# Optimization experiments

Hardware: AMD Instinct MI355X
Metric: run time of the kernel (lower is better)

The kernel has to match this reference:

```python
import jax, jax.numpy as jnp
import numpy as np

D_MODEL = 1024
N_HEADS = 16
D_KV = 64
B, S = 2, 2048


def setup_inputs() -> dict:
    key = jax.random.key(0)
    ks = jax.random.split(key, 7)
    scale = 1.0 / np.sqrt(D_MODEL)
    return {
        "query": jax.random.normal(ks[0], (B, S, D_MODEL), jnp.float32),
        "key": jax.random.normal(ks[1], (B, S, D_MODEL), jnp.float32),
        "value": jax.random.normal(ks[2], (B, S, D_MODEL), jnp.float32),
        "mask": jnp.zeros((B, 1, 1, S), jnp.float32),
        "Wq": jax.random.normal(ks[3], (D_MODEL, N_HEADS * D_KV), jnp.float32) * scale,
        "Wk": jax.random.normal(ks[4], (D_MODEL, N_HEADS * D_KV), jnp.float32) * scale,
        "Wv": jax.random.normal(ks[5], (D_MODEL, N_HEADS * D_KV), jnp.float32) * scale,
        "Wo": jax.random.normal(ks[6], (N_HEADS * D_KV, D_MODEL), jnp.float32) * scale,
    }


def _split_heads(x):
    b, s, _ = x.shape
    return x.reshape(b, s, N_HEADS, D_KV).transpose(0, 2, 1, 3)  # [B,H,S,Dk]


def reference(query, key, value, mask, Wq, Wk, Wv, Wo):
    q = _split_heads(query @ Wq)
    k = _split_heads(key @ Wk)
    v = _split_heads(value @ Wv)
    scores = jnp.einsum("bhqd,bhkd->bhqk", q, k) / jnp.sqrt(
        jnp.asarray(D_KV, scores_dtype := q.dtype)
    )
    scores = scores + mask
    attn = jax.nn.softmax(scores, axis=-1)  # dropout_rate=0 -> identity
    ctx = jnp.einsum("bhqk,bhkd->bhqd", attn, v)
    ctx = ctx.transpose(0, 2, 1, 3).reshape(query.shape[0], -1, N_HEADS * D_KV)
    hidden = ctx @ Wo
    return hidden
```

## Files before the change

kernel.cpp:

```cpp
#include <hip/hip_runtime.h>
#include <hip/hip_bf16.h>
#include <stdint.h>

typedef __bf16 bf16;
typedef __bf16 bf16x8 __attribute__((ext_vector_type(8)));
typedef __bf16 bf16x4 __attribute__((ext_vector_type(4)));
typedef float  f32x4  __attribute__((ext_vector_type(4)));
typedef float  f32x16 __attribute__((ext_vector_type(16)));

#define S_LEN  2048
#define NH     16
#define DKV    64
#define DMODEL 1024
#define LOG2E  1.4426950408889634f

__device__ __forceinline__ void async_load16(const void* g, void* l) {
  __builtin_amdgcn_global_load_lds(
      (const __attribute__((address_space(1))) uint32_t*)(uintptr_t)g,
      (__attribute__((address_space(3))) uint32_t*)(uintptr_t)l,
      16, 0, 0);
}

__global__ void transpose_w(const float* __restrict__ W0, const float* __restrict__ W1,
                            const float* __restrict__ W2, const float* __restrict__ W3,
                            bf16* __restrict__ T0, bf16* __restrict__ T1,
                            bf16* __restrict__ T2, bf16* __restrict__ T3)
{
  int z = blockIdx.z;
  const float* W = (z == 0) ? W0 : (z == 1) ? W1 : (z == 2) ? W2 : W3;
  bf16* T = (z == 0) ? T0 : (z == 1) ? T1 : (z == 2) ? T2 : T3;
  __shared__ float tile[32][33];
  int n0 = blockIdx.x * 32, k0 = blockIdx.y * 32;
  int tx = threadIdx.x, ty = threadIdx.y;
  for (int i = 0; i < 32; i += 8)
    tile[ty + i][tx] = W[(size_t)(k0 + ty + i) * DMODEL + n0 + tx];
  __syncthreads();
  for (int i = 0; i < 32; i += 8)
    T[(size_t)(n0 + ty + i) * DMODEL + k0 + tx] = (bf16)tile[tx][ty + i];
}

__global__ __launch_bounds__(256) void gemm_qkv(
    const float* __restrict__ Aq, const float* __restrict__ Ak, const float* __restrict__ Av,
    const bf16* __restrict__ Bq, const bf16* __restrict__ Bk, const bf16* __restrict__ Bv,
    bf16* __restrict__ Cq, bf16* __restrict__ Ck, bf16* __restrict__ Cv)
{
  __shared__ __align__(16) char smem[64 * 132 * 2];
  bf16* As = (bf16*)smem;
  bf16* Bs = (bf16*)smem + 128 * 32;
  bf16* Ls = (bf16*)smem;

  const int z = blockIdx.z;
  const float* A = (z == 0) ? Aq : (z == 1) ? Ak : Av;
  const bf16* Bt = (z == 0) ? Bq : (z == 1) ? Bk : Bv;
  bf16* C        = (z == 0) ? Cq : (z == 1) ? Ck : Cv;

  const int m0 = blockIdx.x * 128;
  const int n0 = blockIdx.y * 128;
  const int tid = threadIdx.x;
  const int lane = tid & 63;
  const int wave = tid >> 6;
  const int wm = (wave >> 1) * 64;
  const int wn = (wave & 1) * 64;
  const int row = lane & 15;
  const int quad = lane >> 4;

  f32x4 acc[4][4];
  for (int i = 0; i < 4; ++i)
    for (int j = 0; j < 4; ++j) acc[i][j] = (f32x4){0.f, 0.f, 0.f, 0.f};

  const int ar = tid >> 2;
  const int ac8 = (tid & 3) * 8;

  for (int kt = 0; kt < 32; ++kt) {
    const int kk = kt << 5;
    const float* s0p = A + (size_t)(m0 + ar) * DMODEL + kk + ac8;
    const float* s1p = s0p + (size_t)64 * DMODEL;
    f32x4 a00 = *(const f32x4*)s0p;
    f32x4 a01 = *(const f32x4*)(s0p + 4);
    f32x4 a10 = *(const f32x4*)s1p;
    f32x4 a11 = *(const f32x4*)(s1p + 4);
    __syncthreads();
    for (int j = 0; j < 2; ++j) {
      int base = j * 256 + wave * 64;
      int idx = base + lane;
      int r = idx >> 2;
      int cb = (idx & 3) << 4;
      async_load16((const char*)(Bt + (size_t)(n0 + r) * DMODEL + kk) + cb,
                   (char*)Bs + (size_t)base * 16);
    }
    bf16x8 o0, o1;
    for (int u = 0; u < 4; ++u) { o0[u] = (bf16)a00[u]; o0[u + 4] = (bf16)a01[u]; }
    for (int u = 0; u < 4; ++u) { o1[u] = (bf16)a10[u]; o1[u + 4] = (bf16)a11[u]; }
    *(bf16x8*)(As + ar * 32 + ac8) = o0;
    *(bf16x8*)(As + (ar + 64) * 32 + ac8) = o1;
    __syncthreads();
    bf16x8 af[4], bfr[4];
    for (int i = 0; i < 4; ++i)
      af[i] = *(const bf16x8*)(As + (wm + i * 16 + row) * 32 + quad * 8);
    for (int j = 0; j < 4; ++j)
      bfr[j] = *(const bf16x8*)(Bs + (wn + j * 16 + row) * 32 + quad * 8);
    for (int i = 0; i < 4; ++i)
      for (int j = 0; j < 4; ++j)
        acc[i][j] = __builtin_amdgcn_mfma_f32_16x16x32_bf16(af[i], bfr[j], acc[i][j], 0, 0, 0);
  }

  if (z != 2) {
    const int bq = m0 >> 11;
    for (int p = 0; p < 2; ++p) {
      __syncthreads();
      if ((wave >> 1) == p) {
        for (int i = 0; i < 4; ++i)
          for (int j = 0; j < 4; ++j)
            for (int r = 0; r < 4; ++r)
              Ls[(i * 16 + quad * 4 + r) * 132 + wn + j * 16 + row] = (bf16)acc[i][j][r];
      }
      __syncthreads();
      for (int u = 0; u < 4; ++u) {
        int cc = u * 256 + tid;
        int rloc = cc >> 4, c8 = (cc & 15) * 8;
        int s = (m0 + p * 64 + rloc) & 2047;
        int gn = n0 + c8;
        int h = gn >> 6, d = gn & 63;
        bf16x8 val = *(const bf16x8*)(Ls + rloc * 132 + c8);
        *(bf16x8*)(C + (((size_t)(bq * NH + h)) * S_LEN + s) * DKV + d) = val;
      }
    }
  } else {
    for (int i = 0; i < 4; ++i)
      for (int j = 0; j < 4; ++j) {
        int gm = m0 + wm + i * 16 + quad * 4;
        int gn = n0 + wn + j * 16 + row;
        int b = gm >> 11, s = gm & 2047;
        int h = gn >> 6,  d = gn & 63;
        int bh = b * NH + h;
        int tile = s >> 6, kb = (s & 63) >> 2;
        bf16x4 t;
        for (int r = 0; r < 4; ++r) t[r] = (bf16)acc[i][j][r];
        *(bf16x4*)(C + ((((size_t)bh * 32 + tile) * 16 + kb) * 64 + d) * 4) = t;
      }
  }
}

__global__ __launch_bounds__(256, 4) void attn_kernel(
    const bf16* __restrict__ Qh, const bf16* __restrict__ Kh, const bf16* __restrict__ Vperm,
    const float* __restrict__ mask, float* __restrict__ Opart, float* __restrict__ Lpart)
{
  __shared__ __align__(16) bf16 Ks[64 * 64];
  __shared__ __align__(16) bf16 Vts[64 * 64];
  __shared__ __align__(16) float masks2[64];

  const int bh = blockIdx.x;
  const int b = bh >> 4;
  const int q0 = blockIdx.y * 128;
  const int zh = blockIdx.z;
  const int tid = threadIdx.x;
  const int lane = tid & 63;
  const int wave = tid >> 6;
  const int ln = lane & 31;
  const int hi = lane >> 5;
  const float SC2 = 0.125f * LOG2E;

  const int qg = q0 + wave * 32 + ln;
  bf16x8 qf[4];
  {
    const bf16* qrow = Qh + ((size_t)bh * S_LEN + qg) * DKV;
    for (int c = 0; c < 4; ++c)
      qf[c] = *(const bf16x8*)(qrow + c * 16 + hi * 8);
  }

  f32x16 O[2];
  for (int nb = 0; nb < 2; ++nb)
    for (int i = 0; i < 16; ++i) O[nb][i] = 0.f;
  float lsum = 0.f;

  for (int it = 0; it < 16; ++it) {
    const int kv0 = zh * 1024 + it * 64;
    __syncthreads();
    const bf16* vtile = Vperm + ((size_t)bh * 32 + (kv0 >> 6)) * 4096;
    for (int j = 0; j < 2; ++j) {
      int base = j * 256 + wave * 64;
      int idx = base + lane;
      int r = idx >> 3;
      int cc = (idx & 7) ^ (r & 7);
      async_load16(Kh + ((size_t)bh * S_LEN + kv0 + r) * DKV + cc * 8,
                   (char*)Ks + (size_t)base * 16);
      async_load16(vtile + (size_t)idx * 8,
                   (char*)Vts + (size_t)base * 16);
    }
    if (tid < 64) masks2[tid] = mask[b * S_LEN + kv0 + tid] * LOG2E;
    __syncthreads();

    f32x16 Sm[2];
    for (int i = 0; i < 16; ++i) { Sm[0][i] = 0.f; Sm[1][i] = 0.f; }
    for (int c = 0; c < 4; ++c) {
      bf16x8 k0 = *(const bf16x8*)(Ks + ln * 64        + (((2 * c + hi) ^ (ln & 7)) << 3));
      bf16x8 k1 = *(const bf16x8*)(Ks + (32 + ln) * 64 + (((2 * c + hi) ^ (ln & 7)) << 3));
      Sm[0] = __builtin_amdgcn_mfma_f32_32x32x16_bf16(k0, qf[c], Sm[0], 0, 0, 0);
      Sm[1] = __builtin_amdgcn_mfma_f32_32x32x16_bf16(k1, qf[c], Sm[1], 0, 0, 0);
    }

    for (int cg = 0; cg < 4; ++cg) {
      int mb = cg >> 1, g = cg & 1;
      int koff = 32 * mb + 16 * g + 4 * hi;
      f32x4 mklo = *(const f32x4*)(masks2 + koff);
      f32x4 mkhi = *(const f32x4*)(masks2 + koff + 8);
      bf16x8 ap;
      float ls0 = 0.f;
      for (int u = 0; u < 4; ++u) {
        float p = __builtin_amdgcn_exp2f(Sm[mb][g * 8 + u] * SC2 + mklo[u]);
        ls0 += p; ap[u] = (bf16)p;
      }
      for (int u = 0; u < 4; ++u) {
        float p = __builtin_amdgcn_exp2f(Sm[mb][g * 8 + 4 + u] * SC2 + mkhi[u]);
        ls0 += p; ap[4 + u] = (bf16)p;
      }
      lsum += ls0;
      int kb0 = hi + 4 * g + 8 * mb;
      for (int nb = 0; nb < 2; ++nb) {
        int d = nb * 32 + ln;
        bf16x4 lo = *(const bf16x4*)(Vts + ((size_t)kb0 * 64 + d) * 4);
        bf16x4 hv = *(const bf16x4*)(Vts + ((size_t)(kb0 + 2) * 64 + d) * 4);
        bf16x8 bv;
        for (int u = 0; u < 4; ++u) { bv[u] = lo[u]; bv[u + 4] = hv[u]; }
        O[nb] = __builtin_amdgcn_mfma_f32_32x32x16_bf16(ap, bv, O[nb], 0, 0, 0);
      }
    }
  }

  float lt = lsum + __shfl_xor(lsum, 32, 64);
  if (lane < 32)
    Lpart[((size_t)zh * 32 + bh) * S_LEN + q0 + wave * 32 + ln] = lt;

  float* ob = Opart + (((size_t)zh * 32 + bh) * S_LEN) * DKV;
  for (int g = 0; g < 4; ++g)
    for (int nb = 0; nb < 2; ++nb)
      for (int j = 0; j < 4; ++j) {
        int qrow = q0 + wave * 32 + j + 8 * g + 4 * hi;
        ob[(size_t)qrow * DKV + nb * 32 + ln] = O[nb][g * 4 + j];
      }
}

__global__ __launch_bounds__(256) void gemm_out(
    const float* __restrict__ Opart, const float* __restrict__ Lpart,
    const bf16* __restrict__ Wot, float* __restrict__ Cout)
{
  __shared__ __align__(16) bf16 As[64 * 32];
  __shared__ __align__(16) bf16 Bs[128 * 32];
  __shared__ float rinv[NH * 64];

  const int m0 = blockIdx.x * 64;
  const int n0 = blockIdx.y * 128;
  const int tid = threadIdx.x;
  const int lane = tid & 63;
  const int wave = tid >> 6;
  const int wm = (wave >> 1) * 32;
  const int wn = (wave & 1) * 64;
  const int row = lane & 15;
  const int quad = lane >> 4;
  const int b = m0 >> 11;
  const int s0 = m0 & 2047;

  for (int u = 0; u < 4; ++u) {
    int idx = u * 256 + tid;
    int h = idx >> 6, r = idx & 63;
    float l = Lpart[((size_t)(b * NH + h)) * S_LEN + s0 + r]
            + Lpart[((size_t)(32 + b * NH + h)) * S_LEN + s0 + r];
    rinv[idx] = 1.0f / l;
  }

  f32x4 acc[2][4];
  for (int i = 0; i < 2; ++i)
    for (int j = 0; j < 4; ++j) acc[i][j] = (f32x4){0.f, 0.f, 0.f, 0.f};

  const int ar = tid >> 2;
  const int ac8 = (tid & 3) * 8;

  for (int kt = 0; kt < 32; ++kt) {
    const int kk = kt << 5;
    const int h = kk >> 6;
    const int d0 = (kk & 63) + ac8;
    const float* p0 = Opart + (((size_t)(b * NH + h)) * S_LEN + s0 + ar) * DKV + d0;
    const float* p1 = Opart + (((size_t)(32 + b * NH + h)) * S_LEN + s0 + ar) * DKV + d0;
    f32x4 a00 = *(const f32x4*)p0;
    f32x4 a01 = *(const f32x4*)(p0 + 4);
    f32x4 a10 = *(const f32x4*)p1;
    f32x4 a11 = *(const f32x4*)(p1 + 4);
    __syncthreads();
    for (int j = 0; j < 2; ++j) {
      int base = j * 256 + wave * 64;
      int idx = base + lane;
      int r = idx >> 2;
      int cb = (idx & 3) << 4;
      async_load16((const char*)(Wot + (size_t)(n0 + r) * DMODEL + kk) + cb,
                   (char*)Bs + (size_t)base * 16);
    }
    float rv = rinv[h * 64 + ar];
    bf16x8 o;
    for (int u = 0; u < 4; ++u) o[u]     = (bf16)((a00[u] + a10[u]) * rv);
    for (int u = 0; u < 4; ++u) o[u + 4] = (bf16)((a01[u] + a11[u]) * rv);
    *(bf16x8*)(As + ar * 32 + ac8) = o;
    __syncthreads();
    bf16x8 af[2], bfr[4];
    for (int i = 0; i < 2; ++i)
      af[i] = *(const bf16x8*)(As + (wm + i * 16 + row) * 32 + quad * 8);
    for (int j = 0; j < 4; ++j)
      bfr[j] = *(const bf16x8*)(Bs + (wn + j * 16 + row) * 32 + quad * 8);
    for (int i = 0; i < 2; ++i)
      for (int j = 0; j < 4; ++j)
        acc[i][j] = __builtin_amdgcn_mfma_f32_16x16x32_bf16(af[i], bfr[j], acc[i][j], 0, 0, 0);
  }

  for (int i = 0; i < 2; ++i)
    for (int j = 0; j < 4; ++j)
      for (int r = 0; r < 4; ++r) {
        int gm = m0 + wm + i * 16 + quad * 4 + r;
        int gn = n0 + wn + j * 16 + row;
        Cout[(size_t)gm * DMODEL + gn] = acc[i][j][r];
      }
}

extern "C" void kernel_launch(void* const* d_in, const int* in_sizes, int n_in,
                              void* d_out, int out_size, void* d_ws, size_t ws_size,
                              hipStream_t stream)
{
  const float* query = (const float*)d_in[0];
  const float* key_  = (const float*)d_in[1];
  const float* value = (const float*)d_in[2];
  const float* mask  = (const float*)d_in[3];
  const float* Wq = (const float*)d_in[4];
  const float* Wk = (const float*)d_in[5];
  const float* Wv = (const float*)d_in[6];
  const float* Wo = (const float*)d_in[7];

  char* ws = (char*)d_ws;
  const size_t MB = (size_t)1 << 20;
  bf16* qh    = (bf16*)(ws + 0 * MB);
  bf16* kh    = (bf16*)(ws + 8 * MB);
  bf16* vperm = (bf16*)(ws + 16 * MB);
  bf16* wot   = (bf16*)(ws + 24 * MB);
  float* Opart = (float*)(ws + 26 * MB);
  bf16* wqt   = (bf16*)(ws + 26 * MB);
  bf16* wkt   = (bf16*)(ws + 28 * MB);
  bf16* wvt   = (bf16*)(ws + 30 * MB);
  float* Lpart = (float*)(ws + 58 * MB);

  transpose_w<<<dim3(32, 32, 4), dim3(32, 8), 0, stream>>>(Wq, Wk, Wv, Wo, wqt, wkt, wvt, wot);
  gemm_qkv<<<dim3(32, 8, 3), 256, 0, stream>>>(query, key_, value, wqt, wkt, wvt,
                                               qh, kh, vperm);
  attn_kernel<<<dim3(32, 16, 2), 256, 0, stream>>>(qh, kh, vperm, mask, Opart, Lpart);
  gemm_out<<<dim3(64, 8), 256, 0, stream>>>(Opart, Lpart, wot, (float*)d_out);
}
```

Measured before the change: 225.5 us.

## Double GEMM K-tile to 64 with XOR-swizzled LDS and store attention partials as bf16

```diff
diff --git a/kernel.cpp b/kernel.cpp
--- a/kernel.cpp
+++ b/kernel.cpp
@@ -44,9 +44,9 @@
     const bf16* __restrict__ Bq, const bf16* __restrict__ Bk, const bf16* __restrict__ Bv,
     bf16* __restrict__ Cq, bf16* __restrict__ Ck, bf16* __restrict__ Cv)
 {
-  __shared__ __align__(16) char smem[64 * 132 * 2];
+  __shared__ __align__(16) char smem[32768];
   bf16* As = (bf16*)smem;
-  bf16* Bs = (bf16*)smem + 128 * 32;
+  bf16* Bs = (bf16*)smem + 128 * 64;
   bf16* Ls = (bf16*)smem;
 
   const int z = blockIdx.z;
@@ -68,40 +68,47 @@
   for (int i = 0; i < 4; ++i)
     for (int j = 0; j < 4; ++j) acc[i][j] = (f32x4){0.f, 0.f, 0.f, 0.f};
 
-  const int ar = tid >> 2;
-  const int ac8 = (tid & 3) * 8;
-
-  for (int kt = 0; kt < 32; ++kt) {
-    const int kk = kt << 5;
-    const float* s0p = A + (size_t)(m0 + ar) * DMODEL + kk + ac8;
-    const float* s1p = s0p + (size_t)64 * DMODEL;
-    f32x4 a00 = *(const f32x4*)s0p;
-    f32x4 a01 = *(const f32x4*)(s0p + 4);
-    f32x4 a10 = *(const f32x4*)s1p;
-    f32x4 a11 = *(const f32x4*)(s1p + 4);
-    __syncthreads();
-    for (int j = 0; j < 2; ++j) {
+  const int arc = tid & 7;
+  const int arr = tid >> 3;
+
+  for (int kt = 0; kt < 16; ++kt) {
+    const int kk = kt << 6;
+    f32x4 av0[4], av1[4];
+    for (int u = 0; u < 4; ++u) {
+      const float* sp = A + (size_t)(m0 + u * 32 + arr) * DMODEL + kk + arc * 8;
+      av0[u] = *(const f32x4*)sp;
+      av1[u] = *(const f32x4*)(sp + 4);
+    }
+    __syncthreads();
+    for (int j = 0; j < 4; ++j) {
       int base = j * 256 + wave * 64;
       int idx = base + lane;
-      int r = idx >> 2;
-      int cb = (idx & 3) << 4;
-      async_load16((const char*)(Bt + (size_t)(n0 + r) * DMODEL + kk) + cb,
+      int r = idx >> 3;
+      int cc = (idx & 7) ^ (r & 7);
+      async_load16(Bt + (size_t)(n0 + r) * DMODEL + kk + cc * 8,
                    (char*)Bs + (size_t)base * 16);
     }
-    bf16x8 o0, o1;
-    for (int u = 0; u < 4; ++u) { o0[u] = (bf16)a00[u]; o0[u + 4] = (bf16)a01[u]; }
-    for (int u = 0; u < 4; ++u) { o1[u] = (bf16)a10[u]; o1[u + 4] = (bf16)a11[u]; }
-    *(bf16x8*)(As + ar * 32 + ac8) = o0;
-    *(bf16x8*)(As + (ar + 64) * 32 + ac8) = o1;
-    __syncthreads();
-    bf16x8 af[4], bfr[4];
-    for (int i = 0; i < 4; ++i)
-      af[i] = *(const bf16x8*)(As + (wm + i * 16 + row) * 32 + quad * 8);
-    for (int j = 0; j < 4; ++j)
-      bfr[j] = *(const bf16x8*)(Bs + (wn + j * 16 + row) * 32 + quad * 8);
-    for (int i = 0; i < 4; ++i)
-      for (int j = 0; j < 4; ++j)
-        acc[i][j] = __builtin_amdgcn_mfma_f32_16x16x32_bf16(af[i], bfr[j], acc[i][j], 0, 0, 0);
+    for (int u = 0; u < 4; ++u) {
+      bf16x8 o;
+      for (int w = 0; w < 4; ++w) { o[w] = (bf16)av0[u][w]; o[w + 4] = (bf16)av1[u][w]; }
+      int r = u * 32 + arr;
+      *(bf16x8*)(As + r * 64 + ((arc ^ (r & 7)) << 3)) = o;
+    }
+    __syncthreads();
+    for (int ks = 0; ks < 2; ++ks) {
+      bf16x8 af[4], bfr[4];
+      for (int i = 0; i < 4; ++i) {
+        int rr = wm + i * 16 + row;
+        af[i] = *(const bf16x8*)(As + rr * 64 + (((quad + ks * 4) ^ (rr & 7)) << 3));
+      }
+      for (int j = 0; j < 4; ++j) {
+        int rr = wn + j * 16 + row;
+        bfr[j] = *(const bf16x8*)(Bs + rr * 64 + (((quad + ks * 4) ^ (rr & 7)) << 3));
+      }
+      for (int i = 0; i < 4; ++i)
+        for (int j = 0; j < 4; ++j)
+          acc[i][j] = __builtin_amdgcn_mfma_f32_16x16x32_bf16(af[i], bfr[j], acc[i][j], 0, 0, 0);
+    }
   }
 
   if (z != 2) {
@@ -143,7 +150,7 @@
 
 __global__ __launch_bounds__(256, 4) void attn_kernel(
     const bf16* __restrict__ Qh, const bf16* __restrict__ Kh, const bf16* __restrict__ Vperm,
-    const float* __restrict__ mask, float* __restrict__ Opart, float* __restrict__ Lpart)
+    const float* __restrict__ mask, bf16* __restrict__ Opart, float* __restrict__ Lpart)
 {
   __shared__ __align__(16) bf16 Ks[64 * 64];
   __shared__ __align__(16) bf16 Vts[64 * 64];
@@ -231,21 +238,21 @@
   if (lane < 32)
     Lpart[((size_t)zh * 32 + bh) * S_LEN + q0 + wave * 32 + ln] = lt;
 
-  float* ob = Opart + (((size_t)zh * 32 + bh) * S_LEN) * DKV;
+  bf16* ob = Opart + (((size_t)zh * 32 + bh) * S_LEN) * DKV;
   for (int g = 0; g < 4; ++g)
     for (int nb = 0; nb < 2; ++nb)
       for (int j = 0; j < 4; ++j) {
         int qrow = q0 + wave * 32 + j + 8 * g + 4 * hi;
-        ob[(size_t)qrow * DKV + nb * 32 + ln] = O[nb][g * 4 + j];
+        ob[(size_t)qrow * DKV + nb * 32 + ln] = (bf16)O[nb][g * 4 + j];
       }
 }
 
 __global__ __launch_bounds__(256) void gemm_out(
-    const float* __restrict__ Opart, const float* __restrict__ Lpart,
+    const bf16* __restrict__ Opart, const float* __restrict__ Lpart,
     const bf16* __restrict__ Wot, float* __restrict__ Cout)
 {
-  __shared__ __align__(16) bf16 As[64 * 32];
-  __shared__ __align__(16) bf16 Bs[128 * 32];
+  __shared__ __align__(16) bf16 As[64 * 64];
+  __shared__ __align__(16) bf16 Bs[128 * 64];
   __shared__ float rinv[NH * 64];
 
   const int m0 = blockIdx.x * 64;
@@ -272,42 +279,55 @@
   for (int i = 0; i < 2; ++i)
     for (int j = 0; j < 4; ++j) acc[i][j] = (f32x4){0.f, 0.f, 0.f, 0.f};
 
-  const int ar = tid >> 2;
-  const int ac8 = (tid & 3) * 8;
-
-  for (int kt = 0; kt < 32; ++kt) {
-    const int kk = kt << 5;
-    const int h = kk >> 6;
-    const int d0 = (kk & 63) + ac8;
-    const float* p0 = Opart + (((size_t)(b * NH + h)) * S_LEN + s0 + ar) * DKV + d0;
-    const float* p1 = Opart + (((size_t)(32 + b * NH + h)) * S_LEN + s0 + ar) * DKV + d0;
-    f32x4 a00 = *(const f32x4*)p0;
-    f32x4 a01 = *(const f32x4*)(p0 + 4);
-    f32x4 a10 = *(const f32x4*)p1;
-    f32x4 a11 = *(const f32x4*)(p1 + 4);
-    __syncthreads();
-    for (int j = 0; j < 2; ++j) {
+  const int arc = tid & 7;
+  const int arr = tid >> 3;
+
+  for (int kt = 0; kt < 16; ++kt) {
+    const int h = kt;
+    bf16x8 h0[2], h1[2];
+    for (int u = 0; u < 2; ++u) {
+      int r = u * 32 + arr;
+      size_t off = ((size_t)(b * NH + h) * S_LEN + s0 + r) * DKV + arc * 8;
+      h0[u] = *(const bf16x8*)(Opart + off);
+      h1[u] = *(const bf16x8*)(Opart + (size_t)32 * S_LEN * DKV * NH * 2 / NH / 2 * 0 + off + (size_t)32 * NH * 0 + ((size_t)32 * S_LEN * DKV) * 2 * 0);
+    }
+    for (int u = 0; u < 2; ++u) {
+      int r = u * 32 + arr;
+      size_t off = ((size_t)(32 + b * NH + h) * S_LEN + s0 + r) * DKV + arc * 8;
+      h1[u] = *(const bf16x8*)(Opart + off);
+    }
+    __syncthreads();
+    for (int j = 0; j < 4; ++j) {
       int base = j * 256 + wave * 64;
       int idx = base + lane;
-      int r = idx >> 2;
-      int cb = (idx & 3) << 4;
-      async_load16((const char*)(Wot + (size_t)(n0 + r) * DMODEL + kk) + cb,
+      int r = idx >> 3;
+      int cc = (idx & 7) ^ (r & 7);
+      async_load16(Wot + (size_t)(n0 + r) * DMODEL + kt * 64 + cc * 8,
                    (char*)Bs + (size_t)base * 16);
     }
-    float rv = rinv[h * 64 + ar];
-    bf16x8 o;
-    for (int u = 0; u < 4; ++u) o[u]     = (bf16)((a00[u] + a10[u]) * rv);
-    for (int u = 0; u < 4; ++u) o[u + 4] = (bf16)((a01[u] + a11[u]) * rv);
-    *(bf16x8*)(As + ar * 32 + ac8) = o;
-    __syncthreads();
-    bf16x8 af[2], bfr[4];
-    for (int i = 0; i < 2; ++i)
-      af[i] = *(const bf16x8*)(As + (wm + i * 16 + row) * 32 + quad * 8);
-    for (int j = 0; j < 4; ++j)
-      bfr[j] = *(const bf16x8*)(Bs + (wn + j * 16 + row) * 32 + quad * 8);
-    for (int i = 0; i < 2; ++i)
-      for (int j = 0; j < 4; ++j)
-        acc[i][j] = __builtin_amdgcn_mfma_f32_16x16x32_bf16(af[i], bfr[j], acc[i][j], 0, 0, 0);
+    for (int u = 0; u < 2; ++u) {
+      int r = u * 32 + arr;
+      float rv = rinv[h * 64 + r];
+      bf16x8 o;
+      for (int w = 0; w < 8; ++w)
+        o[w] = (bf16)(((float)h0[u][w] + (float)h1[u][w]) * rv);
+      *(bf16x8*)(As + r * 64 + ((arc ^ (r & 7)) << 3)) = o;
+    }
+    __syncthreads();
+    for (int ks = 0; ks < 2; ++ks) {
+      bf16x8 af[2], bfr[4];
+      for (int i = 0; i < 2; ++i) {
+        int rr = wm + i * 16 + row;
+        af[i] = *(const bf16x8*)(As + rr * 64 + (((quad + ks * 4) ^ (rr & 7)) << 3));
+      }
+      for (int j = 0; j < 4; ++j) {
+        int rr = wn + j * 16 + row;
+        bfr[j] = *(const bf16x8*)(Bs + rr * 64 + (((quad + ks * 4) ^ (rr & 7)) << 3));
+      }
+      for (int i = 0; i < 2; ++i)
+        for (int j = 0; j < 4; ++j)
+          acc[i][j] = __builtin_amdgcn_mfma_f32_16x16x32_bf16(af[i], bfr[j], acc[i][j], 0, 0, 0);
+    }
   }
 
   for (int i = 0; i < 2; ++i)
@@ -338,7 +358,7 @@
   bf16* kh    = (bf16*)(ws + 8 * MB);
   bf16* vperm = (bf16*)(ws + 16 * MB);
   bf16* wot   = (bf16*)(ws + 24 * MB);
-  float* Opart = (float*)(ws + 26 * MB);
+  bf16* Opart = (bf16*)(ws + 26 * MB);
   bf16* wqt   = (bf16*)(ws + 26 * MB);
   bf16* wkt   = (bf16*)(ws + 28 * MB);
   bf16* wvt   = (bf16*)(ws + 30 * MB);
```

Result: no change. 221.9 us (-1.6%).

## Double-buffer A tiles, load B fragments from global, store attention partials as bf16

Applied to the files above, without the earlier changes.

```diff
diff --git a/kernel.cpp b/kernel.cpp
--- a/kernel.cpp
+++ b/kernel.cpp
@@ -44,9 +44,8 @@
     const bf16* __restrict__ Bq, const bf16* __restrict__ Bk, const bf16* __restrict__ Bv,
     bf16* __restrict__ Cq, bf16* __restrict__ Ck, bf16* __restrict__ Cv)
 {
-  __shared__ __align__(16) char smem[64 * 132 * 2];
+  __shared__ __align__(16) char smem[16896];
   bf16* As = (bf16*)smem;
-  bf16* Bs = (bf16*)smem + 128 * 32;
   bf16* Ls = (bf16*)smem;
 
   const int z = blockIdx.z;
@@ -70,35 +69,37 @@
 
   const int ar = tid >> 2;
   const int ac8 = (tid & 3) * 8;
+  const float* Ab0 = A + (size_t)(m0 + ar) * DMODEL + ac8;
+  const float* Ab1 = Ab0 + (size_t)64 * DMODEL;
+  const bf16*  Bb  = Bt + (size_t)(n0 + wn + row) * DMODEL + quad * 8;
+
+  f32x4 a00 = *(const f32x4*)(Ab0);
+  f32x4 a01 = *(const f32x4*)(Ab0 + 4);
+  f32x4 a10 = *(const f32x4*)(Ab1);
+  f32x4 a11 = *(const f32x4*)(Ab1 + 4);
 
   for (int kt = 0; kt < 32; ++kt) {
     const int kk = kt << 5;
-    const float* s0p = A + (size_t)(m0 + ar) * DMODEL + kk + ac8;
-    const float* s1p = s0p + (size_t)64 * DMODEL;
-    f32x4 a00 = *(const f32x4*)s0p;
-    f32x4 a01 = *(const f32x4*)(s0p + 4);
-    f32x4 a10 = *(const f32x4*)s1p;
-    f32x4 a11 = *(const f32x4*)(s1p + 4);
-    __syncthreads();
-    for (int j = 0; j < 2; ++j) {
-      int base = j * 256 + wave * 64;
-      int idx = base + lane;
-      int r = idx >> 2;
-      int cb = (idx & 3) << 4;
-      async_load16((const char*)(Bt + (size_t)(n0 + r) * DMODEL + kk) + cb,
-                   (char*)Bs + (size_t)base * 16);
-    }
+    bf16* Ab = As + (kt & 1) * 4096;
     bf16x8 o0, o1;
     for (int u = 0; u < 4; ++u) { o0[u] = (bf16)a00[u]; o0[u + 4] = (bf16)a01[u]; }
     for (int u = 0; u < 4; ++u) { o1[u] = (bf16)a10[u]; o1[u + 4] = (bf16)a11[u]; }
-    *(bf16x8*)(As + ar * 32 + ac8) = o0;
-    *(bf16x8*)(As + (ar + 64) * 32 + ac8) = o1;
+    *(bf16x8*)(Ab + ar * 32 + ac8) = o0;
+    *(bf16x8*)(Ab + (ar + 64) * 32 + ac8) = o1;
     __syncthreads();
-    bf16x8 af[4], bfr[4];
+    if (kt < 31) {
+      const int kn = kk + 32;
+      a00 = *(const f32x4*)(Ab0 + kn);
+      a01 = *(const f32x4*)(Ab0 + kn + 4);
+      a10 = *(const f32x4*)(Ab1 + kn);
+      a11 = *(const f32x4*)(Ab1 + kn + 4);
+    }
+    bf16x8 bfr[4];
+    for (int j = 0; j < 4; ++j)
+      bfr[j] = *(const bf16x8*)(Bb + (size_t)j * 16 * DMODEL + kk);
+    bf16x8 af[4];
     for (int i = 0; i < 4; ++i)
-      af[i] = *(const bf16x8*)(As + (wm + i * 16 + row) * 32 + quad * 8);
-    for (int j = 0; j < 4; ++j)
-      bfr[j] = *(const bf16x8*)(Bs + (wn + j * 16 + row) * 32 + quad * 8);
+      af[i] = *(const bf16x8*)(Ab + (wm + i * 16 + row) * 32 + quad * 8);
     for (int i = 0; i < 4; ++i)
       for (int j = 0; j < 4; ++j)
         acc[i][j] = __builtin_amdgcn_mfma_f32_16x16x32_bf16(af[i], bfr[j], acc[i][j], 0, 0, 0);
@@ -143,7 +144,7 @@
 
 __global__ __launch_bounds__(256, 4) void attn_kernel(
     const bf16* __restrict__ Qh, const bf16* __restrict__ Kh, const bf16* __restrict__ Vperm,
-    const float* __restrict__ mask, float* __restrict__ Opart, float* __restrict__ Lpart)
+    const float* __restrict__ mask, bf16* __restrict__ Opart, float* __restrict__ Lpart)
 {
   __shared__ __align__(16) bf16 Ks[64 * 64];
   __shared__ __align__(16) bf16 Vts[64 * 64];
@@ -231,21 +232,20 @@
   if (lane < 32)
     Lpart[((size_t)zh * 32 + bh) * S_LEN + q0 + wave * 32 + ln] = lt;
 
-  float* ob = Opart + (((size_t)zh * 32 + bh) * S_LEN) * DKV;
+  bf16* ob = Opart + (((size_t)zh * 32 + bh) * S_LEN) * DKV;
   for (int g = 0; g < 4; ++g)
     for (int nb = 0; nb < 2; ++nb)
       for (int j = 0; j < 4; ++j) {
         int qrow = q0 + wave * 32 + j + 8 * g + 4 * hi;
-        ob[(size_t)qrow * DKV + nb * 32 + ln] = O[nb][g * 4 + j];
+        ob[(size_t)qrow * DKV + nb * 32 + ln] = (bf16)O[nb][g * 4 + j];
       }
 }
 
 __global__ __launch_bounds__(256) void gemm_out(
-    const float* __restrict__ Opart, const float* __restrict__ Lpart,
+    const bf16* __restrict__ Opart, const float* __restrict__ Lpart,
     const bf16* __restrict__ Wot, float* __restrict__ Cout)
 {
-  __shared__ __align__(16) bf16 As[64 * 32];
-  __shared__ __align__(16) bf16 Bs[128 * 32];
+  __shared__ __align__(16) bf16 As[2][64 * 32];
   __shared__ float rinv[NH * 64];
 
   const int m0 = blockIdx.x * 64;
@@ -267,6 +267,7 @@
             + Lpart[((size_t)(32 + b * NH + h)) * S_LEN + s0 + r];
     rinv[idx] = 1.0f / l;
   }
+  __syncthreads();
 
   f32x4 acc[2][4];
   for (int i = 0; i < 2; ++i)
@@ -274,37 +275,34 @@
 
   const int ar = tid >> 2;
   const int ac8 = (tid & 3) * 8;
+  const bf16* Bb = Wot + (size_t)(n0 + wn + row) * DMODEL + quad * 8;
+
+  bf16x8 h0 = *(const bf16x8*)(Opart + ((size_t)(b * NH) * S_LEN + s0 + ar) * DKV + ac8);
+  bf16x8 h1 = *(const bf16x8*)(Opart + ((size_t)(32 + b * NH) * S_LEN + s0 + ar) * DKV + ac8);
 
   for (int kt = 0; kt < 32; ++kt) {
     const int kk = kt << 5;
     const int h = kk >> 6;
-    const int d0 = (kk & 63) + ac8;
-    const float* p0 = Opart + (((size_t)(b * NH + h)) * S_LEN + s0 + ar) * DKV + d0;
-    const float* p1 = Opart + (((size_t)(32 + b * NH + h)) * S_LEN + s0 + ar) * DKV + d0;
-    f32x4 a00 = *(const f32x4*)p0;
-    f32x4 a01 = *(const f32x4*)(p0 + 4);
-    f32x4 a10 = *(const f32x4*)p1;
-    f32x4 a11 = *(const f32x4*)(p1 + 4);
-    __syncthreads();
-    for (int j = 0; j < 2; ++j) {
-      int base = j * 256 + wave * 64;
-      int idx = base + lane;
-      int r = idx >> 2;
-      int cb = (idx & 3) << 4;
-      async_load16((const char*)(Wot + (size_t)(n0 + r) * DMODEL + kk) + cb,
-                   (char*)Bs + (size_t)base * 16);
-    }
+    bf16* Ab = As[kt & 1];
     float rv = rinv[h * 64 + ar];
     bf16x8 o;
-    for (int u = 0; u < 4; ++u) o[u]     = (bf16)((a00[u] + a10[u]) * rv);
-    for (int u = 0; u < 4; ++u) o[u + 4] = (bf16)((a01[u] + a11[u]) * rv);
-    *(bf16x8*)(As + ar * 32 + ac8) = o;
+    for (int w = 0; w < 8; ++w)
+      o[w] = (bf16)(((float)h0[w] + (float)h1[w]) * rv);
+    *(bf16x8*)(Ab + ar * 32 + ac8) = o;
     __syncthreads();
-    bf16x8 af[2], bfr[4];
+    if (kt < 31) {
+      const int kn = kk + 32;
+      const int hn = kn >> 6;
+      const int dn = (kn & 63) + ac8;
+      h0 = *(const bf16x8*)(Opart + ((size_t)(b * NH + hn) * S_LEN + s0 + ar) * DKV + dn);
+      h1 = *(const bf16x8*)(Opart + ((size_t)(32 + b * NH + hn) * S_LEN + s0 + ar) * DKV + dn);
+    }
+    bf16x8 bfr[4];
+    for (int j = 0; j < 4; ++j)
+      bfr[j] = *(const bf16x8*)(Bb + (size_t)j * 16 * DMODEL + kk);
+    bf16x8 af[2];
     for (int i = 0; i < 2; ++i)
-      af[i] = *(const bf16x8*)(As + (wm + i * 16 + row) * 32 + quad * 8);
-    for (int j = 0; j < 4; ++j)
-      bfr[j] = *(const bf16x8*)(Bs + (wn + j * 16 + row) * 32 + quad * 8);
+      af[i] = *(const bf16x8*)(Ab + (wm + i * 16 + row) * 32 + quad * 8);
     for (int i = 0; i < 2; ++i)
       for (int j = 0; j < 4; ++j)
         acc[i][j] = __builtin_amdgcn_mfma_f32_16x16x32_bf16(af[i], bfr[j], acc[i][j], 0, 0, 0);
@@ -338,7 +336,7 @@
   bf16* kh    = (bf16*)(ws + 8 * MB);
   bf16* vperm = (bf16*)(ws + 16 * MB);
   bf16* wot   = (bf16*)(ws + 24 * MB);
-  float* Opart = (float*)(ws + 26 * MB);
+  bf16* Opart = (bf16*)(ws + 26 * MB);
   bf16* wqt   = (bf16*)(ws + 26 * MB);
   bf16* wkt   = (bf16*)(ws + 28 * MB);
   bf16* wvt   = (bf16*)(ws + 30 * MB);
```

After: 253.7 us. +12.5%, slower.
